# Kernel optimization log

Hardware: AMD Instinct MI355X
Metric: run time of the kernel (lower is better)

## Reference

```python
import jax, jax.numpy as jnp
import numpy as np

B, L, ENC, DEC, ATT = 256, 196, 2048, 512, 512

def setup_inputs() -> dict:
    key = jax.random.key(0)
    ks = jax.random.split(key, 8)
    s_enc = 1.0 / np.sqrt(ENC); s_dec = 1.0 / np.sqrt(DEC); s_att = 1.0 / np.sqrt(ATT)
    return {
        "encoder_out": jax.random.normal(ks[0], (B, L, ENC), dtype=jnp.float32),
        "decoder_hidden": jax.random.normal(ks[1], (B, DEC), dtype=jnp.float32),
        "W_enc": jax.random.uniform(ks[2], (ENC, ATT), jnp.float32, -s_enc, s_enc),
        "b_enc": jax.random.uniform(ks[3], (ATT,), jnp.float32, -s_enc, s_enc),
        "W_dec": jax.random.uniform(ks[4], (DEC, ATT), jnp.float32, -s_dec, s_dec),
        "b_dec": jax.random.uniform(ks[5], (ATT,), jnp.float32, -s_dec, s_dec),
        "W_att": jax.random.uniform(ks[6], (ATT, 1), jnp.float32, -s_att, s_att),
        "b_att": jax.random.uniform(ks[7], (1,), jnp.float32, -s_att, s_att),
    }

def reference(encoder_out, decoder_hidden, W_enc, b_enc, W_dec, b_dec, W_att, b_att):
    # encoder_att: [B, L, A]; decoder_att: [B, A]
    encoder_att = jnp.einsum('ble,ea->bla', encoder_out, W_enc) + b_enc
    decoder_att = decoder_hidden @ W_dec + b_dec
    hidden = jax.nn.relu(encoder_att + decoder_att[:, None, :])  # [B, L, A]
    att = jnp.einsum('bla,a->bl', hidden, W_att[:, 0]) + b_att[0]  # [B, L]
    alpha = jax.nn.softmax(att, axis=1)  # softmax over sequence dim
    awe = jnp.einsum('ble,bl->be', encoder_out, alpha)  # weighted sum
    return awe, alpha
```

## Files before the change

### kernel.cpp

```cpp
#include <hip/hip_runtime.h>
#include <hip/hip_bf16.h>
#include <stdint.h>

#define NB 256
#define NL 196
#define NE 2048
#define ND 512
#define NA 512
#define NM (NB * NL)

#define BPCOPY (1u << 20)

typedef __attribute__((ext_vector_type(4))) float f32x4;
typedef __attribute__((ext_vector_type(8))) short bf16x8;

static __device__ __forceinline__ unsigned short f2bf(float f) {
  __hip_bfloat16 h = __float2bfloat16(f);
  unsigned short u;
  __builtin_memcpy(&u, &h, 2);
  return u;
}

__global__ __launch_bounds__(512) void k_prep(
    const float* __restrict__ W, unsigned short* __restrict__ Bp,
    const float* __restrict__ dec, const float* __restrict__ Wd,
    const float* __restrict__ bd, const float* __restrict__ be,
    float* __restrict__ d2) {
  if (blockIdx.x < 256) {
    int t = blockIdx.x * 512 + threadIdx.x;
    int lane = t & 63;
    int kt32 = (t >> 6) & 63;
    int ntile = t >> 12;
    int col = ntile * 16 + (lane & 15);
    int k0 = kt32 * 32 + ((lane >> 4) << 3);
    bf16x8 o;
#pragma unroll
    for (int j = 0; j < 8; ++j) o[j] = (short)f2bf(W[(size_t)(k0 + j) * NA + col]);
#pragma unroll
    for (int x = 0; x < 8; ++x)
      *reinterpret_cast<bf16x8*>(Bp + (size_t)x * BPCOPY + ((size_t)t << 3)) = o;
  } else {
    __shared__ float dh[8][ND];
    const int b0 = (blockIdx.x - 256) * 8, tid = threadIdx.x;
#pragma unroll
    for (int j = 0; j < 8; ++j) dh[j][tid] = dec[(size_t)(b0 + j) * ND + tid];
    __syncthreads();
    float base = bd[tid] + be[tid];
    float acc[8];
#pragma unroll
    for (int j = 0; j < 8; ++j) acc[j] = base;
#pragma unroll 4
    for (int e = 0; e < ND; ++e) {
      float w = Wd[(size_t)e * NA + tid];
#pragma unroll
      for (int j = 0; j < 8; ++j) acc[j] = fmaf(dh[j][e], w, acc[j]);
    }
#pragma unroll
    for (int j = 0; j < 8; ++j) d2[(size_t)(b0 + j) * NA + tid] = acc[j];
  }
}

#define BM 128
#define BK 64
#define KT (NE / BK)

__global__ __launch_bounds__(512, 2) void k_main(
    const float* __restrict__ A,
    const unsigned short* __restrict__ Bp,
    const float* __restrict__ d2,
    const float* __restrict__ Watt,
    const float* __restrict__ batt,
    float* __restrict__ att)
{
  __shared__ unsigned short As[2][BM * BK];
  __shared__ float att_w[8][BM];

  const int tid = threadIdx.x;
  const int lane = tid & 63;
  const int wid = tid >> 6;
  const int lq = lane >> 4;
  const int lr = lane & 15;
  const int row0 = blockIdx.x * BM;

  f32x4 acc[8][4];
#pragma unroll
  for (int mf = 0; mf < 8; ++mf)
#pragma unroll
    for (int r = 0; r < 4; ++r) {
      int rowg = row0 + mf * 16 + lq * 4 + r;
      int bb = rowg / NL;
      const float* d2r = d2 + (size_t)bb * NA + wid * 64 + lr;
#pragma unroll
      for (int nf = 0; nf < 4; ++nf) acc[mf][nf][r] = d2r[nf * 16];
    }

  const int srow = tid >> 2;
  const int sg = tid & 3;
  const float* ag = A + (size_t)(row0 + srow) * NE + sg * 16;
  const int wo0 = srow * BK + (((sg * 2) ^ (srow & 7)) << 3);
  const int wo1 = srow * BK + (((sg * 2 + 1) ^ (srow & 7)) << 3);

  f32x4 s0, s1, s2, s3;
  auto cvt_store = [&](int buf) {
    bf16x8 o0, o1;
#pragma unroll
    for (int j = 0; j < 4; ++j) {
      o0[j] = (short)f2bf(s0[j]); o0[j + 4] = (short)f2bf(s1[j]);
      o1[j] = (short)f2bf(s2[j]); o1[j + 4] = (short)f2bf(s3[j]);
    }
    *reinterpret_cast<bf16x8*>(&As[buf][wo0]) = o0;
    *reinterpret_cast<bf16x8*>(&As[buf][wo1]) = o1;
  };

  s0 = *reinterpret_cast<const f32x4*>(ag);
  s1 = *reinterpret_cast<const f32x4*>(ag + 4);
  s2 = *reinterpret_cast<const f32x4*>(ag + 8);
  s3 = *reinterpret_cast<const f32x4*>(ag + 12);
  cvt_store(0);
  __syncthreads();

  const unsigned short* bpw = Bp + (size_t)(blockIdx.x & 7) * BPCOPY
                                 + (size_t)(wid * 4) * 32768 + lane * 8;

  for (int kt = 0; kt < KT; ++kt) {
    const int cur = kt & 1;
    bf16x8 bf[2][4];
#pragma unroll
    for (int ks = 0; ks < 2; ++ks)
#pragma unroll
      for (int nf = 0; nf < 4; ++nf)
        bf[ks][nf] = *reinterpret_cast<const bf16x8*>(bpw + (size_t)nf * 32768 + (size_t)(kt * 2 + ks) * 512);
    if (kt + 1 < KT) {
      const float* agn = ag + (size_t)(kt + 1) * BK;
      s0 = *reinterpret_cast<const f32x4*>(agn);
      s1 = *reinterpret_cast<const f32x4*>(agn + 4);
      s2 = *reinterpret_cast<const f32x4*>(agn + 8);
      s3 = *reinterpret_cast<const f32x4*>(agn + 12);
    }
#pragma unroll
    for (int ks = 0; ks < 2; ++ks)
#pragma unroll
      for (int mf = 0; mf < 8; ++mf) {
        const int rrow = mf * 16 + lr;
        const int chunk = (ks * 4 + lq) ^ (lr & 7);
        bf16x8 af = *reinterpret_cast<const bf16x8*>(&As[cur][rrow * BK + (chunk << 3)]);
#pragma unroll
        for (int nf = 0; nf < 4; ++nf)
          acc[mf][nf] = __builtin_amdgcn_mfma_f32_16x16x32_bf16(af, bf[ks][nf], acc[mf][nf], 0, 0, 0);
      }
    if (kt + 1 < KT) cvt_store(cur ^ 1);
    __syncthreads();
  }

  float w[4];
#pragma unroll
  for (int nf = 0; nf < 4; ++nf) w[nf] = Watt[wid * 64 + nf * 16 + lr];
#pragma unroll
  for (int mf = 0; mf < 8; ++mf)
#pragma unroll
    for (int r = 0; r < 4; ++r) {
      float s = 0.f;
#pragma unroll
      for (int nf = 0; nf < 4; ++nf) s = fmaf(fmaxf(acc[mf][nf][r], 0.f), w[nf], s);
      s += __shfl_xor(s, 1);
      s += __shfl_xor(s, 2);
      s += __shfl_xor(s, 4);
      s += __shfl_xor(s, 8);
      if (lr == 0) att_w[wid][mf * 16 + lq * 4 + r] = s;
    }
  __syncthreads();
  if (tid < BM) {
    float s = 0.f;
#pragma unroll
    for (int wv = 0; wv < 8; ++wv) s += att_w[wv][tid];
    att[row0 + tid] = s + batt[0];
  }
}

__global__ __launch_bounds__(256) void k_awe(
    const float* __restrict__ enc, const float* __restrict__ att,
    float* __restrict__ alpha_out, float* __restrict__ awe) {
  __shared__ float al[256];
  const int b = blockIdx.x >> 1, ch = blockIdx.x & 1, tid = threadIdx.x;

  if (tid < 64) {
    const int lane = tid;
    const float* ar = att + (size_t)b * NL;
    float v[4];
#pragma unroll
    for (int i = 0; i < 4; ++i) {
      int l = i * 64 + lane;
      v[i] = (l < NL) ? ar[l] : -1e30f;
    }
    float m = fmaxf(fmaxf(v[0], v[1]), fmaxf(v[2], v[3]));
#pragma unroll
    for (int o = 32; o >= 1; o >>= 1) m = fmaxf(m, __shfl_xor(m, o));
    float e[4];
    float s = 0.f;
#pragma unroll
    for (int i = 0; i < 4; ++i) {
      int l = i * 64 + lane;
      e[i] = (l < NL) ? __expf(v[i] - m) : 0.f;
      s += e[i];
    }
#pragma unroll
    for (int o = 32; o >= 1; o >>= 1) s += __shfl_xor(s, o);
    float inv = 1.f / s;
#pragma unroll
    for (int i = 0; i < 4; ++i) {
      int l = i * 64 + lane;
      if (l < NL) {
        float a = e[i] * inv;
        al[l] = a;
        if (ch == 0) alpha_out[(size_t)b * NL + l] = a;
      }
    }
  }
  __syncthreads();

  const float* ep = enc + (size_t)b * NL * NE + ch * 1024 + tid * 4;
  f32x4 a0 = {0.f, 0.f, 0.f, 0.f}, a1 = a0, a2 = a0, a3 = a0;
#pragma unroll 2
  for (int l = 0; l < NL; l += 4) {
    f32x4 v0 = *reinterpret_cast<const f32x4*>(ep + (size_t)l * NE);
    f32x4 v1 = *reinterpret_cast<const f32x4*>(ep + (size_t)(l + 1) * NE);
    f32x4 v2 = *reinterpret_cast<const f32x4*>(ep + (size_t)(l + 2) * NE);
    f32x4 v3 = *reinterpret_cast<const f32x4*>(ep + (size_t)(l + 3) * NE);
    float c0 = al[l], c1 = al[l + 1], c2 = al[l + 2], c3 = al[l + 3];
#pragma unroll
    for (int j = 0; j < 4; ++j) {
      a0[j] = fmaf(c0, v0[j], a0[j]);
      a1[j] = fmaf(c1, v1[j], a1[j]);
      a2[j] = fmaf(c2, v2[j], a2[j]);
      a3[j] = fmaf(c3, v3[j], a3[j]);
    }
  }
  f32x4 s4;
#pragma unroll
  for (int j = 0; j < 4; ++j) s4[j] = (a0[j] + a1[j]) + (a2[j] + a3[j]);
  *reinterpret_cast<f32x4*>(awe + (size_t)b * NE + ch * 1024 + tid * 4) = s4;
}

extern "C" void kernel_launch(void* const* d_in, const int* in_sizes, int n_in,
                              void* d_out, int out_size, void* d_ws, size_t ws_size,
                              hipStream_t stream) {
  const float* enc  = (const float*)d_in[0];
  const float* dec  = (const float*)d_in[1];
  const float* Wenc = (const float*)d_in[2];
  const float* benc = (const float*)d_in[3];
  const float* Wdec = (const float*)d_in[4];
  const float* bdec = (const float*)d_in[5];
  const float* Watt = (const float*)d_in[6];
  const float* batt = (const float*)d_in[7];

  float* awe   = (float*)d_out;
  float* alpha = (float*)d_out + (size_t)NB * NE;

  char* ws = (char*)d_ws;
  unsigned short* Bp = (unsigned short*)ws;
  float* d2  = (float*)(ws + (size_t)16 * 1024 * 1024);
  float* att = (float*)(ws + (size_t)16 * 1024 * 1024 + 512 * 1024);

  k_prep<<<dim3(288), dim3(512), 0, stream>>>(Wenc, Bp, dec, Wdec, bdec, benc, d2);
  k_main<<<dim3(NM / BM), dim3(512), 0, stream>>>(enc, Bp, d2, Watt, batt, att);
  k_awe<<<dim3(NB * 2), dim3(256), 0, stream>>>(enc, att, alpha, awe);
}
```

Before: 302.3 us.

## Split attention GEMM across column halves with smaller row tiles, sum partials in softmax

The main GEMM kernel now uses 64-row tiles with 256 threads. Each row tile is split across two workgroups, one per half of the attention dimension. Each workgroup writes a partial attention score, and the softmax kernel adds the two partials. This quadruples the number of workgroups, for better load balance and occupancy across the CUs. In exchange, each encoder row tile is loaded and converted by two workgroups, which doubles global traffic unless caches absorb it. The bias b_att is dropped because softmax is invariant to a constant shift. The weighted-sum kernel is merged into one 512-thread block per batch.

```diff
diff --git a/kernel.cpp b/kernel.cpp
--- a/kernel.cpp
+++ b/kernel.cpp
@@ -60,45 +60,48 @@
   }
 }
 
-#define BM 128
+#define BM 64
 #define BK 64
 #define KT (NE / BK)
 
-__global__ __launch_bounds__(512, 2) void k_main(
+__global__ __launch_bounds__(256, 4) void k_main(
     const float* __restrict__ A,
     const unsigned short* __restrict__ Bp,
     const float* __restrict__ d2,
     const float* __restrict__ Watt,
-    const float* __restrict__ batt,
-    float* __restrict__ att)
+    float* __restrict__ att_part)
 {
   __shared__ unsigned short As[2][BM * BK];
-  __shared__ float att_w[8][BM];
+  __shared__ float att_w[4][BM];
 
   const int tid = threadIdx.x;
   const int lane = tid & 63;
   const int wid = tid >> 6;
   const int lq = lane >> 4;
   const int lr = lane & 15;
-  const int row0 = blockIdx.x * BM;
-
-  f32x4 acc[8][4];
-#pragma unroll
-  for (int mf = 0; mf < 8; ++mf)
+  const int wgid = blockIdx.x;
+  const int ch = wgid & 1;
+  const int rowt = wgid >> 1;
+  const int row0 = rowt * BM;
+  const int col0 = ch * 256 + wid * 64;
+
+  f32x4 acc[4][4];
+#pragma unroll
+  for (int mf = 0; mf < 4; ++mf)
 #pragma unroll
     for (int r = 0; r < 4; ++r) {
       int rowg = row0 + mf * 16 + lq * 4 + r;
       int bb = rowg / NL;
-      const float* d2r = d2 + (size_t)bb * NA + wid * 64 + lr;
+      const float* d2r = d2 + (size_t)bb * NA + col0 + lr;
 #pragma unroll
       for (int nf = 0; nf < 4; ++nf) acc[mf][nf][r] = d2r[nf * 16];
     }
 
   const int srow = tid >> 2;
-  const int sg = tid & 3;
-  const float* ag = A + (size_t)(row0 + srow) * NE + sg * 16;
-  const int wo0 = srow * BK + (((sg * 2) ^ (srow & 7)) << 3);
-  const int wo1 = srow * BK + (((sg * 2 + 1) ^ (srow & 7)) << 3);
+  const int scb = (tid & 3) * 2;
+  const float* ag = A + (size_t)(row0 + srow) * NE + scb * 8;
+  const int wo0 = srow * BK + ((scb ^ (srow & 7)) << 3);
+  const int wo1 = srow * BK + (((scb + 1) ^ (srow & 7)) << 3);
 
   f32x4 s0, s1, s2, s3;
   auto cvt_store = [&](int buf) {
@@ -119,8 +122,8 @@
   cvt_store(0);
   __syncthreads();
 
-  const unsigned short* bpw = Bp + (size_t)(blockIdx.x & 7) * BPCOPY
-                                 + (size_t)(wid * 4) * 32768 + lane * 8;
+  const unsigned short* bpw = Bp + (size_t)(wgid & 7) * BPCOPY
+                                 + (size_t)(ch * 16 + wid * 4) * 32768 + lane * 8;
 
   for (int kt = 0; kt < KT; ++kt) {
     const int cur = kt & 1;
@@ -140,7 +143,7 @@
 #pragma unroll
     for (int ks = 0; ks < 2; ++ks)
 #pragma unroll
-      for (int mf = 0; mf < 8; ++mf) {
+      for (int mf = 0; mf < 4; ++mf) {
         const int rrow = mf * 16 + lr;
         const int chunk = (ks * 4 + lq) ^ (lr & 7);
         bf16x8 af = *reinterpret_cast<const bf16x8*>(&As[cur][rrow * BK + (chunk << 3)]);
@@ -154,9 +157,9 @@
 
   float w[4];
 #pragma unroll
-  for (int nf = 0; nf < 4; ++nf) w[nf] = Watt[wid * 64 + nf * 16 + lr];
-#pragma unroll
-  for (int mf = 0; mf < 8; ++mf)
+  for (int nf = 0; nf < 4; ++nf) w[nf] = Watt[col0 + nf * 16 + lr];
+#pragma unroll
+  for (int mf = 0; mf < 4; ++mf)
 #pragma unroll
     for (int r = 0; r < 4; ++r) {
       float s = 0.f;
@@ -170,27 +173,26 @@
     }
   __syncthreads();
   if (tid < BM) {
-    float s = 0.f;
-#pragma unroll
-    for (int wv = 0; wv < 8; ++wv) s += att_w[wv][tid];
-    att[row0 + tid] = s + batt[0];
-  }
-}
-
-__global__ __launch_bounds__(256) void k_awe(
-    const float* __restrict__ enc, const float* __restrict__ att,
+    float s = att_w[0][tid] + att_w[1][tid] + att_w[2][tid] + att_w[3][tid];
+    att_part[(size_t)ch * NM + row0 + tid] = s;
+  }
+}
+
+__global__ __launch_bounds__(512) void k_awe(
+    const float* __restrict__ enc, const float* __restrict__ att_part,
     float* __restrict__ alpha_out, float* __restrict__ awe) {
   __shared__ float al[256];
-  const int b = blockIdx.x >> 1, ch = blockIdx.x & 1, tid = threadIdx.x;
+  const int b = blockIdx.x, tid = threadIdx.x;
 
   if (tid < 64) {
     const int lane = tid;
-    const float* ar = att + (size_t)b * NL;
+    const float* a0 = att_part + (size_t)b * NL;
+    const float* a1 = att_part + (size_t)NM + (size_t)b * NL;
     float v[4];
 #pragma unroll
     for (int i = 0; i < 4; ++i) {
       int l = i * 64 + lane;
-      v[i] = (l < NL) ? ar[l] : -1e30f;
+      v[i] = (l < NL) ? (a0[l] + a1[l]) : -1e30f;
     }
     float m = fmaxf(fmaxf(v[0], v[1]), fmaxf(v[2], v[3]));
 #pragma unroll
@@ -212,13 +214,13 @@
       if (l < NL) {
         float a = e[i] * inv;
         al[l] = a;
-        if (ch == 0) alpha_out[(size_t)b * NL + l] = a;
+        alpha_out[(size_t)b * NL + l] = a;
       }
     }
   }
   __syncthreads();
 
-  const float* ep = enc + (size_t)b * NL * NE + ch * 1024 + tid * 4;
+  const float* ep = enc + (size_t)b * NL * NE + tid * 4;
   f32x4 a0 = {0.f, 0.f, 0.f, 0.f}, a1 = a0, a2 = a0, a3 = a0;
 #pragma unroll 2
   for (int l = 0; l < NL; l += 4) {
@@ -238,7 +240,7 @@
   f32x4 s4;
 #pragma unroll
   for (int j = 0; j < 4; ++j) s4[j] = (a0[j] + a1[j]) + (a2[j] + a3[j]);
-  *reinterpret_cast<f32x4*>(awe + (size_t)b * NE + ch * 1024 + tid * 4) = s4;
+  *reinterpret_cast<f32x4*>(awe + (size_t)b * NE + tid * 4) = s4;
 }
 
 extern "C" void kernel_launch(void* const* d_in, const int* in_sizes, int n_in,
@@ -251,7 +253,6 @@
   const float* Wdec = (const float*)d_in[4];
   const float* bdec = (const float*)d_in[5];
   const float* Watt = (const float*)d_in[6];
-  const float* batt = (const float*)d_in[7];
 
   float* awe   = (float*)d_out;
   float* alpha = (float*)d_out + (size_t)NB * NE;
@@ -262,6 +263,6 @@
   float* att = (float*)(ws + (size_t)16 * 1024 * 1024 + 512 * 1024);
 
   k_prep<<<dim3(288), dim3(512), 0, stream>>>(Wenc, Bp, dec, Wdec, bdec, benc, d2);
-  k_main<<<dim3(NM / BM), dim3(512), 0, stream>>>(enc, Bp, d2, Watt, batt, att);
-  k_awe<<<dim3(NB * 2), dim3(256), 0, stream>>>(enc, att, alpha, awe);
-}
+  k_main<<<dim3((NM / BM) * 2), dim3(256), 0, stream>>>(enc, Bp, d2, Watt, att);
+  k_awe<<<dim3(NB), dim3(512), 0, stream>>>(enc, att, alpha, awe);
+}
```

Result: slower. 342.1 us (+13.2%).
